# Optimization experiments

Measured on AMD Instinct MI355X. Metric: run time of the kernel, lower is better.

Reference implementation:

```python
import jax, jax.numpy as jnp
import numpy as np
from jax import lax

KS = 3
N = KS * KS


def _conv(x, W, b, pad, stride):
    out = lax.conv_general_dilated(
        x, W, window_strides=(stride, stride),
        padding=[(pad, pad), (pad, pad)],
        dimension_numbers=("NCHW", "OIHW", "NCHW"))
    return out + b[None, :, None, None]


def setup_inputs() -> dict:
    key = jax.random.key(0)
    ks = jax.random.split(key, 5)
    b, c, h, w, outc = 16, 64, 64, 64, 128
    return {
        "x": jax.random.normal(ks[0], (b, c, h, w), jnp.float32),
        "W_off": jax.random.normal(ks[1], (2 * N, c, KS, KS), jnp.float32) * 0.05,
        "b_off": jax.random.normal(ks[2], (2 * N,), jnp.float32) * 0.05,
        "W_k": jax.random.normal(ks[3], (outc, c, KS, KS), jnp.float32) * 0.05,
        "b_k": jax.random.normal(ks[4], (outc,), jnp.float32) * 0.05,
    }


def _deform_conv(x, W_off, b_off, W_k, b_k):
    b, c, h, w = x.shape
    offset = _conv(x, W_off, b_off, pad=1, stride=1)  # [b, 2N, h, w]

    # kernel-grid offsets, flattened with x (row) index first: n = i*ks + j
    rng = jnp.arange(KS, dtype=x.dtype) - (KS - 1) // 2  # [-1, 0, 1]
    pnx = jnp.repeat(rng, KS)  # [N]
    pny = jnp.tile(rng, KS)    # [N]

    # sampling positions p = p0 + p_n + offset, clamped into the image
    px = jnp.arange(h, dtype=x.dtype)[None, None, :, None] + pnx[None, :, None, None] + offset[:, :N]
    py = jnp.arange(w, dtype=x.dtype)[None, None, None, :] + pny[None, :, None, None] + offset[:, N:]
    px = jnp.clip(px, 0, h - 1)
    py = jnp.clip(py, 0, w - 1)

    fx = jnp.floor(px)
    fy = jnp.floor(py)
    tx = px - fx  # fractional parts (bilinear weights)
    ty = py - fy
    x0 = fx.astype(jnp.int32)
    y0 = fy.astype(jnp.int32)
    x1 = jnp.minimum(x0 + 1, h - 1)  # out-of-range tap carries zero weight
    y1 = jnp.minimum(y0 + 1, w - 1)

    x_hw = x.transpose(0, 2, 3, 1).reshape(b, h * w, c)  # [b, hw, c]

    def gather(ix, iy):
        idx = (ix * w + iy).reshape(b, -1, 1)  # [b, N*h*w, 1]
        return jnp.take_along_axis(x_hw, idx, axis=1).reshape(b, N, h, w, c)

    wx0, wx1 = (1 - tx)[..., None], tx[..., None]
    wy0, wy1 = (1 - ty)[..., None], ty[..., None]
    # 4-tap bilinear interpolation == the original's sparse G @ x
    xo = (gather(x0, y0) * wx0 * wy0 + gather(x1, y0) * wx1 * wy0
          + gather(x0, y1) * wx0 * wy1 + gather(x1, y1) * wx1 * wy1)  # [b,N,h,w,c]

    # _reshape_x_offset: out[b,c, i_h*ks+i, i_w*ks+j] = xo[b, i*ks+j, i_h, i_w, c]
    xo = xo.reshape(b, KS, KS, h, w, c).transpose(0, 5, 3, 1, 4, 2)
    xo = xo.reshape(b, c, h * KS, w * KS)

    return _conv(xo, W_k, b_k, pad=0, stride=KS)  # [b, outc, h, w]


def reference(x, W_off, b_off, W_k, b_k):
    return _deform_conv(x, W_off, b_off, W_k, b_k)
```

## Files before the change

kernel.cpp:

```cpp
#include <hip/hip_runtime.h>

typedef __attribute__((ext_vector_type(8))) short bf16x8;
typedef __attribute__((ext_vector_type(4))) float floatx4;

__device__ __forceinline__ unsigned short f2bf(float f) {
    unsigned int u = __float_as_uint(f);
    u += 0x7FFFu + ((u >> 16) & 1u);
    return (unsigned short)(u >> 16);
}

__device__ __forceinline__ int interp_word(int a00, int a01, int a10, int a11,
                                           float w00, float w01, float w10, float w11) {
    float vl = w00 * __uint_as_float((unsigned)a00 << 16)
             + w01 * __uint_as_float((unsigned)a01 << 16)
             + w10 * __uint_as_float((unsigned)a10 << 16)
             + w11 * __uint_as_float((unsigned)a11 << 16);
    float vh = w00 * __uint_as_float((unsigned)a00 & 0xffff0000u)
             + w01 * __uint_as_float((unsigned)a01 & 0xffff0000u)
             + w10 * __uint_as_float((unsigned)a10 & 0xffff0000u)
             + w11 * __uint_as_float((unsigned)a11 & 0xffff0000u);
    return (int)__builtin_amdgcn_perm(__float_as_uint(vh) + 0x8000u,
                                      __float_as_uint(vl) + 0x8000u, 0x07060302u);
}

__device__ __forceinline__ void g2l16(const unsigned short* g, unsigned short* l) {
    __builtin_amdgcn_global_load_lds(
        (const __attribute__((address_space(1))) unsigned int*)g,
        (__attribute__((address_space(3))) unsigned int*)l, 16, 0, 0);
}

__global__ __launch_bounds__(256) void prep_all(const float* __restrict__ x,
        const float* __restrict__ Wk, const float* __restrict__ Woff,
        unsigned short* __restrict__ xt, unsigned short* __restrict__ Wkb2,
        unsigned short* __restrict__ Woffb) {
    int bb = blockIdx.x;
    if (bb < 1024) {
        __shared__ float tile[64][65];
        int b = bb >> 6, y = bb & 63;
        const float* src = x + (size_t)b * 262144 + y * 64;
        int tx = threadIdx.x & 15, tg = threadIdx.x >> 4;
#pragma unroll
        for (int i = 0; i < 4; i++) {
            int c = tg + i * 16;
            float4 v = *(const float4*)(src + (size_t)c * 4096 + tx * 4);
            tile[c][tx * 4 + 0] = v.x; tile[c][tx * 4 + 1] = v.y;
            tile[c][tx * 4 + 2] = v.z; tile[c][tx * 4 + 3] = v.w;
        }
        __syncthreads();
        unsigned short* dst = xt + (size_t)bb * 4096;
#pragma unroll
        for (int i = 0; i < 4; i++) {
            int xc = tg + i * 16;
            int c4 = tx * 4;
            ushort4 v;
            v.x = f2bf(tile[c4 + 0][xc]); v.y = f2bf(tile[c4 + 1][xc]);
            v.z = f2bf(tile[c4 + 2][xc]); v.w = f2bf(tile[c4 + 3][xc]);
            *(ushort4*)(dst + xc * 64 + c4) = v;
        }
    } else if (bb < 1312) {
        int idx = (bb - 1024) * 256 + threadIdx.x;
        int tap = idx >> 13;
        int r = idx & 8191;
        int tile = r >> 9;
        int ln = (r >> 3) & 63;
        int j = r & 7;
        int mt = tile >> 1, kc = tile & 1;
        int oc = mt * 16 + (ln & 15);
        int c = kc * 32 + (ln >> 4) * 8 + j;
        Wkb2[idx] = f2bf(Wk[(oc * 64 + c) * 9 + tap]);
    } else {
        int idx = (bb - 1312) * 256 + threadIdx.x;
        int tap = idx >> 11;
        int r = idx & 2047;
        int tile = r >> 9;
        int ln = (r >> 3) & 63;
        int j = r & 7;
        int mt = tile >> 1, kc = tile & 1;
        int n = mt * 16 + (ln & 15);
        int c = kc * 32 + (ln >> 4) * 8 + j;
        float v = (n < 18) ? Woff[(n * 64 + c) * 9 + tap] : 0.f;
        Woffb[idx] = f2bf(v);
    }
}

__global__ __launch_bounds__(256, 3) void fused_kernel(
        const unsigned short* __restrict__ xt,
        const unsigned short* __restrict__ Wkb2,
        const unsigned short* __restrict__ Woffb,
        const float* __restrict__ boff,
        const float* __restrict__ bias,
        float* __restrict__ out) {
    __shared__ unsigned short As0[8192];
    __shared__ unsigned short As1[8192];
    __shared__ float offs[64][20];
    int tid = threadIdx.x;
    int wave = tid >> 6, lane = tid & 63;
    int frow = lane & 15, quad = lane >> 4;
    int bb = blockIdx.x;
    int xcd = bb & 7, idx = bb >> 3;
    int b = xcd * 2 + (idx >> 6);
    int pxBase = (idx & 63) * 64;
    int pl = wave * 16 + frow;
    int px = pxBase + pl;
    int y = px >> 6, xx = px & 63;
    const char* img = (const char*)(xt + (size_t)b * 262144) + quad * 16;

    float bv[2][4];
#pragma unroll
    for (int mt = 0; mt < 2; mt++)
#pragma unroll
        for (int rg = 0; rg < 4; rg++) {
            int n = mt * 16 + quad * 4 + rg;
            bv[mt][rg] = (n < 18) ? boff[n] : 0.f;
        }

    floatx4 acc1[2];
    acc1[0] = (floatx4)(0.f); acc1[1] = (floatx4)(0.f);
#pragma unroll
    for (int tap = 0; tap < 9; tap++) {
        int ry = y + tap / 3 - 1, rx = xx + tap % 3 - 1;
        bool valid = (ry >= 0) & (ry < 64) & (rx >= 0) & (rx < 64);
        const char* src = img + ((ry * 64 + rx) << 7);
        const unsigned short* wofft = Woffb + tap * 2048 + lane * 8;
        bf16x8 bz = {};
#pragma unroll
        for (int kc = 0; kc < 2; kc++) {
            bf16x8 bfr = valid ? *(const bf16x8*)(src + kc * 64) : bz;
#pragma unroll
            for (int mt = 0; mt < 2; mt++) {
                bf16x8 af = *(const bf16x8*)(wofft + (mt * 2 + kc) * 512);
                acc1[mt] = __builtin_amdgcn_mfma_f32_16x16x32_bf16(af, bfr, acc1[mt], 0, 0, 0);
            }
        }
    }
#pragma unroll
    for (int mt = 0; mt < 2; mt++)
#pragma unroll
        for (int rg = 0; rg < 4; rg++) {
            int n = mt * 16 + quad * 4 + rg;
            if (n < 18) offs[pl][n] = acc1[mt][rg] + bv[mt][rg];
        }

    floatx4 acc[8];
#pragma unroll
    for (int i = 0; i < 8; i++) acc[i] = (floatx4)(0.f);

    const float* op = &offs[pl][0];

    auto stage = [&](int tap, int4 (&r00)[2], int4 (&r01)[2], int4 (&r10)[2],
                     int4 (&r11)[2], floatx4& w) {
        float orow = op[tap];
        float ocol = op[9 + tap];
        float pr = (float)(y + tap / 3 - 1) + orow;
        float pc = (float)(xx + tap % 3 - 1) + ocol;
        pr = fminf(fmaxf(pr, 0.f), 63.f);
        pc = fminf(fmaxf(pc, 0.f), 63.f);
        float fr = floorf(pr), fc = floorf(pc);
        float tr = pr - fr, tc = pc - fc;
        int r0 = (int)fr, c0 = (int)fc;
        int r1 = min(r0 + 1, 63), c1 = min(c0 + 1, 63);
        w[0] = (1.f - tr) * (1.f - tc);
        w[1] = (1.f - tr) * tc;
        w[2] = tr * (1.f - tc);
        w[3] = tr * tc;
        const char* p00 = img + ((r0 * 64 + c0) << 7);
        const char* p01 = img + ((r0 * 64 + c1) << 7);
        const char* p10 = img + ((r1 * 64 + c0) << 7);
        const char* p11 = img + ((r1 * 64 + c1) << 7);
#pragma unroll
        for (int kc = 0; kc < 2; kc++) {
            r00[kc] = *(const int4*)(p00 + kc * 64);
            r01[kc] = *(const int4*)(p01 + kc * 64);
            r10[kc] = *(const int4*)(p10 + kc * 64);
            r11[kc] = *(const int4*)(p11 + kc * 64);
        }
    };

    auto makeB = [&](int4 (&a00)[2], int4 (&a01)[2], int4 (&a10)[2], int4 (&a11)[2],
                     floatx4& w, bf16x8& b0, bf16x8& b1) {
#pragma unroll
        for (int kc = 0; kc < 2; kc++) {
            int4 r;
            r.x = interp_word(a00[kc].x, a01[kc].x, a10[kc].x, a11[kc].x, w[0], w[1], w[2], w[3]);
            r.y = interp_word(a00[kc].y, a01[kc].y, a10[kc].y, a11[kc].y, w[0], w[1], w[2], w[3]);
            r.z = interp_word(a00[kc].z, a01[kc].z, a10[kc].z, a11[kc].z, w[0], w[1], w[2], w[3]);
            r.w = interp_word(a00[kc].w, a01[kc].w, a10[kc].w, a11[kc].w, w[0], w[1], w[2], w[3]);
            if (kc == 0) b0 = __builtin_bit_cast(bf16x8, r);
            else         b1 = __builtin_bit_cast(bf16x8, r);
        }
    };

    int4 c00[2], c01[2], c10[2], c11[2];
    int4 n00[2], n01[2], n10[2], n11[2];
    floatx4 cw, nw;

#define STAGE_A(BUF, TAP) do {                                                 \
        const unsigned short* gs_ = Wkb2 + (TAP) * 8192 + wave * 2048 + lane * 8; \
        g2l16(gs_,         &BUF[wave * 2048]);                                 \
        g2l16(gs_ + 512,   &BUF[wave * 2048 + 512]);                           \
        g2l16(gs_ + 1024,  &BUF[wave * 2048 + 1024]);                          \
        g2l16(gs_ + 1536,  &BUF[wave * 2048 + 1536]);                          \
    } while (0)

#define BODY(TAP, RBUF, WBUF, LAST) do {                                       \
        asm volatile("s_waitcnt vmcnt(8)\n\ts_barrier" ::: "memory");          \
        if (!(LAST)) { STAGE_A(WBUF, (TAP) + 1); }                             \
        __builtin_amdgcn_sched_barrier(0);                                     \
        if (!(LAST)) stage((TAP) + 1, n00, n01, n10, n11, nw);                 \
        __builtin_amdgcn_sched_barrier(0);                                     \
        bf16x8 bf0, bf1;                                                       \
        makeB(c00, c01, c10, c11, cw, bf0, bf1);                               \
        _Pragma("unroll")                                                      \
        for (int mt = 0; mt < 8; mt++) {                                       \
            bf16x8 af = *(const bf16x8*)&RBUF[(mt * 2) * 512 + lane * 8];      \
            acc[mt] = __builtin_amdgcn_mfma_f32_16x16x32_bf16(af, bf0, acc[mt], 0, 0, 0); \
        }                                                                      \
        _Pragma("unroll")                                                      \
        for (int mt = 0; mt < 8; mt++) {                                       \
            bf16x8 af = *(const bf16x8*)&RBUF[(mt * 2 + 1) * 512 + lane * 8];  \
            acc[mt] = __builtin_amdgcn_mfma_f32_16x16x32_bf16(af, bf1, acc[mt], 0, 0, 0); \
        }                                                                      \
        if (!(LAST)) {                                                         \
            _Pragma("unroll")                                                  \
            for (int kc = 0; kc < 2; kc++) {                                   \
                c00[kc] = n00[kc]; c01[kc] = n01[kc];                          \
                c10[kc] = n10[kc]; c11[kc] = n11[kc];                          \
            }                                                                  \
            cw = nw;                                                           \
        }                                                                      \
    } while (0)

    __builtin_amdgcn_sched_barrier(0);
    STAGE_A(As0, 0);
    __builtin_amdgcn_sched_barrier(0);
    stage(0, c00, c01, c10, c11, cw);

#pragma unroll 1
    for (int t2 = 0; t2 < 4; t2++) {
        int tap = t2 * 2;
        BODY(tap,     As0, As1, false);
        BODY(tap + 1, As1, As0, false);
    }
    BODY(8, As0, As1, true);

#undef BODY
#undef STAGE_A

    float* outb = out + (size_t)b * 524288 + px;
#pragma unroll
    for (int mt = 0; mt < 8; mt++) {
        float4 bc = *(const float4*)(bias + mt * 16 + quad * 4);
        float bcv[4] = {bc.x, bc.y, bc.z, bc.w};
#pragma unroll
        for (int rg = 0; rg < 4; rg++) {
            int oc = mt * 16 + quad * 4 + rg;
            outb[oc * 4096] = acc[mt][rg] + bcv[rg];
        }
    }
}

extern "C" void kernel_launch(void* const* d_in, const int* in_sizes, int n_in,
                              void* d_out, int out_size, void* d_ws, size_t ws_size,
                              hipStream_t stream) {
    const float* x    = (const float*)d_in[0];
    const float* Woff = (const float*)d_in[1];
    const float* boff = (const float*)d_in[2];
    const float* Wk   = (const float*)d_in[3];
    const float* bk   = (const float*)d_in[4];
    float* out = (float*)d_out;

    char* ws = (char*)d_ws;
    unsigned short* xt    = (unsigned short*)ws;
    unsigned short* Wkb2  = (unsigned short*)(ws + 8388608);
    unsigned short* Woffb = (unsigned short*)(ws + 8536064);

    prep_all<<<1384, 256, 0, stream>>>(x, Wk, Woff, xt, Wkb2, Woffb);
    fused_kernel<<<1024, 256, 0, stream>>>(xt, Wkb2, Woffb, boff, bk, out);
}
```

Baseline: 134.2 us.

## Split fused deform-conv into sampler and GEMM kernels with workspace intermediate

Unfuses the offset-conv plus bilinear sampling from the main GEMM. A sampler kernel writes interpolated bf16 columns to a workspace buffer, and a separate GEMM kernel consumes them with 32-pixel tiles per wave, double-buffering both A and B. The aim is to take the gather/interp latency off the MFMA loop and let the GEMM reuse each weight fragment across two N tiles. In exchange it adds a large intermediate write and read (about 75 MB across all images) and more launches if the workspace is small. It falls back to the old fused kernel when the workspace is insufficient.

```diff
diff --git a/kernel.cpp b/kernel.cpp
--- a/kernel.cpp
+++ b/kernel.cpp
@@ -83,7 +83,196 @@
     }
 }
 
-__global__ __launch_bounds__(256, 3) void fused_kernel(
+__global__ __launch_bounds__(256, 4) void sampler_kernel(
+        const unsigned short* __restrict__ xt,
+        const unsigned short* __restrict__ Woffb,
+        const float* __restrict__ boff,
+        unsigned short* __restrict__ xo,
+        int b0, int chunkpx) {
+    __shared__ float offs[64][20];
+    int tid = threadIdx.x;
+    int wave = tid >> 6, lane = tid & 63;
+    int frow = lane & 15, quad = lane >> 4;
+    int nwg = gridDim.x;
+    int bb = (blockIdx.x & 7) * (nwg >> 3) + (blockIdx.x >> 3);
+    int bLoc = bb >> 6;
+    int b = b0 + bLoc;
+    int pxBase = (bb & 63) * 64;
+    int pl = wave * 16 + frow;
+    int px = pxBase + pl;
+    int y = px >> 6, xx = px & 63;
+    const char* img = (const char*)(xt + (size_t)b * 262144) + quad * 16;
+
+    float bv[2][4];
+#pragma unroll
+    for (int mt = 0; mt < 2; mt++)
+#pragma unroll
+        for (int rg = 0; rg < 4; rg++) {
+            int n = mt * 16 + quad * 4 + rg;
+            bv[mt][rg] = (n < 18) ? boff[n] : 0.f;
+        }
+
+    floatx4 acc1[2];
+    acc1[0] = (floatx4)(0.f); acc1[1] = (floatx4)(0.f);
+#pragma unroll
+    for (int tap = 0; tap < 9; tap++) {
+        int ry = y + tap / 3 - 1, rx = xx + tap % 3 - 1;
+        bool valid = (ry >= 0) & (ry < 64) & (rx >= 0) & (rx < 64);
+        const char* src = img + ((ry * 64 + rx) << 7);
+        const unsigned short* wofft = Woffb + tap * 2048 + lane * 8;
+        bf16x8 bz = {};
+#pragma unroll
+        for (int kc = 0; kc < 2; kc++) {
+            bf16x8 bfr = valid ? *(const bf16x8*)(src + kc * 64) : bz;
+#pragma unroll
+            for (int mt = 0; mt < 2; mt++) {
+                bf16x8 af = *(const bf16x8*)(wofft + (mt * 2 + kc) * 512);
+                acc1[mt] = __builtin_amdgcn_mfma_f32_16x16x32_bf16(af, bfr, acc1[mt], 0, 0, 0);
+            }
+        }
+    }
+#pragma unroll
+    for (int mt = 0; mt < 2; mt++)
+#pragma unroll
+        for (int rg = 0; rg < 4; rg++) {
+            int n = mt * 16 + quad * 4 + rg;
+            if (n < 18) offs[pl][n] = acc1[mt][rg] + bv[mt][rg];
+        }
+
+    const float* op = &offs[pl][0];
+
+#pragma unroll 1
+    for (int tap = 0; tap < 9; tap++) {
+        float orow = op[tap];
+        float ocol = op[9 + tap];
+        float pr = (float)(y + tap / 3 - 1) + orow;
+        float pc = (float)(xx + tap % 3 - 1) + ocol;
+        pr = fminf(fmaxf(pr, 0.f), 63.f);
+        pc = fminf(fmaxf(pc, 0.f), 63.f);
+        float fr = floorf(pr), fc = floorf(pc);
+        float tr = pr - fr, tc = pc - fc;
+        int r0 = (int)fr, c0 = (int)fc;
+        int r1 = min(r0 + 1, 63), c1 = min(c0 + 1, 63);
+        float w00 = (1.f - tr) * (1.f - tc);
+        float w01 = (1.f - tr) * tc;
+        float w10 = tr * (1.f - tc);
+        float w11 = tr * tc;
+        const char* p00 = img + ((r0 * 64 + c0) << 7);
+        const char* p01 = img + ((r0 * 64 + c1) << 7);
+        const char* p10 = img + ((r1 * 64 + c0) << 7);
+        const char* p11 = img + ((r1 * 64 + c1) << 7);
+        int4 g00[2], g01[2], g10[2], g11[2];
+#pragma unroll
+        for (int kc = 0; kc < 2; kc++) {
+            g00[kc] = *(const int4*)(p00 + kc * 64);
+            g01[kc] = *(const int4*)(p01 + kc * 64);
+            g10[kc] = *(const int4*)(p10 + kc * 64);
+            g11[kc] = *(const int4*)(p11 + kc * 64);
+        }
+        unsigned short* dst = xo + (size_t)(tap * chunkpx + bLoc * 4096 + px) * 64 + quad * 8;
+#pragma unroll
+        for (int kc = 0; kc < 2; kc++) {
+            int4 r;
+            r.x = interp_word(g00[kc].x, g01[kc].x, g10[kc].x, g11[kc].x, w00, w01, w10, w11);
+            r.y = interp_word(g00[kc].y, g01[kc].y, g10[kc].y, g11[kc].y, w00, w01, w10, w11);
+            r.z = interp_word(g00[kc].z, g01[kc].z, g10[kc].z, g11[kc].z, w00, w01, w10, w11);
+            r.w = interp_word(g00[kc].w, g01[kc].w, g10[kc].w, g11[kc].w, w00, w01, w10, w11);
+            *(bf16x8*)(dst + kc * 32) = __builtin_bit_cast(bf16x8, r);
+        }
+    }
+}
+
+__global__ __launch_bounds__(256, 3) void gemm_kernel(
+        const unsigned short* __restrict__ xo,
+        const unsigned short* __restrict__ Wkb2,
+        const float* __restrict__ bias,
+        float* __restrict__ out,
+        int b0, int chunkpx) {
+    __shared__ unsigned short As0[8192];
+    __shared__ unsigned short As1[8192];
+    int tid = threadIdx.x;
+    int wave = tid >> 6, lane = tid & 63;
+    int frow = lane & 15, quad = lane >> 4;
+    int nwg = gridDim.x;
+    int bb = (blockIdx.x & 7) * (nwg >> 3) + (blockIdx.x >> 3);
+    int P = bb * 128 + wave * 32;
+
+    floatx4 acc[8][2];
+#pragma unroll
+    for (int mt = 0; mt < 8; mt++) { acc[mt][0] = (floatx4)(0.f); acc[mt][1] = (floatx4)(0.f); }
+
+    const unsigned short* bbase = xo + (size_t)(P + frow) * 64 + quad * 8;
+
+    bf16x8 bcur[2][2], bnxt[2][2];
+#define LOAD_B(DST, TAP) do {                                                   \
+        const unsigned short* p_ = bbase + (size_t)(TAP) * chunkpx * 64;        \
+        DST[0][0] = *(const bf16x8*)(p_);                                       \
+        DST[0][1] = *(const bf16x8*)(p_ + 32);                                  \
+        DST[1][0] = *(const bf16x8*)(p_ + 1024);                                \
+        DST[1][1] = *(const bf16x8*)(p_ + 1056);                                \
+    } while (0)
+
+#define STAGE_A(BUF, TAP) do {                                                  \
+        const unsigned short* gs_ = Wkb2 + (TAP) * 8192 + wave * 2048 + lane * 8; \
+        g2l16(gs_,        &BUF[wave * 2048]);                                   \
+        g2l16(gs_ + 512,  &BUF[wave * 2048 + 512]);                             \
+        g2l16(gs_ + 1024, &BUF[wave * 2048 + 1024]);                            \
+        g2l16(gs_ + 1536, &BUF[wave * 2048 + 1536]);                            \
+    } while (0)
+
+#define BODY(TAP, RBUF, WBUF, LAST) do {                                        \
+        asm volatile("s_waitcnt vmcnt(4)\n\ts_barrier" ::: "memory");           \
+        if (!(LAST)) { STAGE_A(WBUF, (TAP) + 1); LOAD_B(bnxt, (TAP) + 1); }     \
+        __builtin_amdgcn_sched_barrier(0);                                      \
+        _Pragma("unroll")                                                       \
+        for (int kc = 0; kc < 2; kc++)                                          \
+            _Pragma("unroll")                                                   \
+            for (int mt = 0; mt < 8; mt++) {                                    \
+                bf16x8 af = *(const bf16x8*)&RBUF[(mt * 2 + kc) * 512 + lane * 8]; \
+                acc[mt][0] = __builtin_amdgcn_mfma_f32_16x16x32_bf16(af, bcur[0][kc], acc[mt][0], 0, 0, 0); \
+                acc[mt][1] = __builtin_amdgcn_mfma_f32_16x16x32_bf16(af, bcur[1][kc], acc[mt][1], 0, 0, 0); \
+            }                                                                   \
+        if (!(LAST)) {                                                          \
+            _Pragma("unroll")                                                   \
+            for (int nt = 0; nt < 2; nt++) {                                    \
+                bcur[nt][0] = bnxt[nt][0]; bcur[nt][1] = bnxt[nt][1];           \
+            }                                                                   \
+        }                                                                       \
+    } while (0)
+
+    STAGE_A(As0, 0);
+    LOAD_B(bcur, 0);
+
+#pragma unroll 1
+    for (int t2 = 0; t2 < 4; t2++) {
+        int tap = t2 * 2;
+        BODY(tap,     As0, As1, false);
+        BODY(tap + 1, As1, As0, false);
+    }
+    BODY(8, As0, As1, true);
+
+#undef BODY
+#undef STAGE_A
+#undef LOAD_B
+
+    int b = b0 + (P >> 12);
+    int pxi = P & 4095;
+    float* outb = out + (size_t)b * 524288 + pxi + frow;
+#pragma unroll
+    for (int mt = 0; mt < 8; mt++) {
+        float4 bc = *(const float4*)(bias + mt * 16 + quad * 4);
+        float bcv[4] = {bc.x, bc.y, bc.z, bc.w};
+#pragma unroll
+        for (int nt = 0; nt < 2; nt++)
+#pragma unroll
+            for (int rg = 0; rg < 4; rg++) {
+                int oc = mt * 16 + quad * 4 + rg;
+                outb[oc * 4096 + nt * 16] = acc[mt][nt][rg] + bcv[rg];
+            }
+    }
+}
+
+__global__ __launch_bounds__(256, 3) void fused_fallback(
         const unsigned short* __restrict__ xt,
         const unsigned short* __restrict__ Wkb2,
         const unsigned short* __restrict__ Woffb,
@@ -113,7 +302,6 @@
             int n = mt * 16 + quad * 4 + rg;
             bv[mt][rg] = (n < 18) ? boff[n] : 0.f;
         }
-
     floatx4 acc1[2];
     acc1[0] = (floatx4)(0.f); acc1[1] = (floatx4)(0.f);
 #pragma unroll
@@ -140,13 +328,10 @@
             int n = mt * 16 + quad * 4 + rg;
             if (n < 18) offs[pl][n] = acc1[mt][rg] + bv[mt][rg];
         }
-
     floatx4 acc[8];
 #pragma unroll
     for (int i = 0; i < 8; i++) acc[i] = (floatx4)(0.f);
-
     const float* op = &offs[pl][0];
-
     auto stage = [&](int tap, int4 (&r00)[2], int4 (&r01)[2], int4 (&r10)[2],
                      int4 (&r11)[2], floatx4& w) {
         float orow = op[tap];
@@ -175,7 +360,6 @@
             r11[kc] = *(const int4*)(p11 + kc * 64);
         }
     };
-
     auto makeB = [&](int4 (&a00)[2], int4 (&a01)[2], int4 (&a10)[2], int4 (&a11)[2],
                      floatx4& w, bf16x8& b0, bf16x8& b1) {
 #pragma unroll
@@ -189,11 +373,9 @@
             else         b1 = __builtin_bit_cast(bf16x8, r);
         }
     };
-
     int4 c00[2], c01[2], c10[2], c11[2];
     int4 n00[2], n01[2], n10[2], n11[2];
     floatx4 cw, nw;
-
 #define STAGE_A(BUF, TAP) do {                                                 \
         const unsigned short* gs_ = Wkb2 + (TAP) * 8192 + wave * 2048 + lane * 8; \
         g2l16(gs_,         &BUF[wave * 2048]);                                 \
@@ -201,7 +383,6 @@
         g2l16(gs_ + 1024,  &BUF[wave * 2048 + 1024]);                          \
         g2l16(gs_ + 1536,  &BUF[wave * 2048 + 1536]);                          \
     } while (0)
-
 #define BODY(TAP, RBUF, WBUF, LAST) do {                                       \
         asm volatile("s_waitcnt vmcnt(8)\n\ts_barrier" ::: "memory");          \
         if (!(LAST)) { STAGE_A(WBUF, (TAP) + 1); }                             \
@@ -229,12 +410,10 @@
             cw = nw;                                                           \
         }                                                                      \
     } while (0)
-
     __builtin_amdgcn_sched_barrier(0);
     STAGE_A(As0, 0);
     __builtin_amdgcn_sched_barrier(0);
     stage(0, c00, c01, c10, c11, cw);
-
 #pragma unroll 1
     for (int t2 = 0; t2 < 4; t2++) {
         int tap = t2 * 2;
@@ -242,10 +421,8 @@
         BODY(tap + 1, As1, As0, false);
     }
     BODY(8, As0, As1, true);
-
 #undef BODY
 #undef STAGE_A
-
     float* outb = out + (size_t)b * 524288 + px;
 #pragma unroll
     for (int mt = 0; mt < 8; mt++) {
@@ -273,7 +450,23 @@
     unsigned short* xt    = (unsigned short*)ws;
     unsigned short* Wkb2  = (unsigned short*)(ws + 8388608);
     unsigned short* Woffb = (unsigned short*)(ws + 8536064);
+    const size_t base = 8572928;
+    unsigned short* xo    = (unsigned short*)(ws + base);
 
     prep_all<<<1384, 256, 0, stream>>>(x, Wk, Woff, xt, Wkb2, Woffb);
-    fused_kernel<<<1024, 256, 0, stream>>>(xt, Wkb2, Woffb, boff, bk, out);
-}
+
+    const size_t per_img = (size_t)9 * 4096 * 64 * 2;
+    int G = 0;
+    for (int g = 16; g >= 1; g >>= 1)
+        if (ws_size >= base + (size_t)g * per_img) { G = g; break; }
+
+    if (G == 0) {
+        fused_fallback<<<1024, 256, 0, stream>>>(xt, Wkb2, Woffb, boff, bk, out);
+        return;
+    }
+    int chunkpx = G * 4096;
+    for (int b0 = 0; b0 < 16; b0 += G) {
+        sampler_kernel<<<G * 64, 256, 0, stream>>>(xt, Woffb, boff, xo, b0, chunkpx);
+        gemm_kernel<<<G * 32, 256, 0, stream>>>(xo, Wkb2, bk, out, b0, chunkpx);
+    }
+}
```

Result: slower. 144.6 us (+7.7%).
